# Optimization experiments

Hardware: AMD Instinct MI355X
Metric: run time of the kernel (lower is better)

The kernel has to match this reference:

```python
import jax, jax.numpy as jnp
from jax import lax
import numpy as np

COMMITMENT = 0.25

def conv(x, w, b, stride, pad):
    # x: NCHW, w: OIHW
    y = lax.conv_general_dilated(x, w, (stride, stride), [(pad, pad), (pad, pad)],
                                 dimension_numbers=('NCHW', 'OIHW', 'NCHW'))
    return y + b[None, :, None, None]

def up2(x):
    # PyTorch nn.Upsample(scale_factor=2, mode='bilinear', align_corners=False)
    b, c, h, w = x.shape
    return jax.image.resize(x, (b, c, 2 * h, 2 * w), method='bilinear')

def vq(z, emb):
    # z: (B, D, H, W); emb: (K, D)
    zc = jnp.transpose(z, (0, 2, 3, 1))          # b h w d
    sh = zc.shape
    flat = zc.reshape(-1, sh[-1])                # (N, D)
    dist = (jnp.sum(flat ** 2, axis=1, keepdims=True)
            + jnp.sum(emb ** 2, axis=1)
            - 2.0 * flat @ emb.T)                # (N, K)
    idx = jnp.argmin(dist, axis=1)               # (N,)
    q = emb[idx].reshape(sh)                     # gather == one-hot @ emb
    e_loss = (lax.stop_gradient(q) - zc) ** 2
    q_loss = (q - lax.stop_gradient(zc)) ** 2
    loss = q_loss + COMMITMENT * e_loss          # (b, h, w, d)
    q_st = zc + lax.stop_gradient(q - zc)        # straight-through
    return jnp.transpose(q_st, (0, 3, 1, 2)), loss

def setup_inputs() -> dict:
    key = jax.random.key(0)
    ks = jax.random.split(key, 32)
    S, K, D, IC = 64, 1024, 64, 3
    def w(k, shape, scale=0.05):
        return jax.random.normal(k, shape, jnp.float32) * scale
    z = lambda n: jnp.zeros((n,), jnp.float32)
    return {
        'x': jax.random.normal(ks[0], (8, IC, 256, 256), jnp.float32),
        'ew1': w(ks[1], (S, IC, 3, 3)),        'eb1': z(S),
        'ew2': w(ks[2], (2 * S, S, 3, 3)),     'eb2': z(2 * S),
        'ew3': w(ks[3], (4 * S, 2 * S, 3, 3)), 'eb3': z(4 * S),
        'ew4': w(ks[4], (8 * S, 4 * S, 3, 3)), 'eb4': z(8 * S),
        'pqw': w(ks[5], (D, 8 * S, 1, 1)),     'pqb': z(D),
        'emb': jax.random.uniform(ks[6], (K, D), jnp.float32, -1.0 / K, 1.0 / K),
        'poqw': w(ks[7], (8 * S, D, 1, 1)),    'poqb': z(8 * S),
        'dw1': w(ks[8], (8 * S, 8 * S, 3, 3)), 'db1': z(8 * S),
        'dw2': w(ks[9], (4 * S, 8 * S, 3, 3)), 'db2': z(4 * S),
        'dw3': w(ks[10], (2 * S, 4 * S, 3, 3)),'db3': z(2 * S),
        'dw4': w(ks[11], (S, 2 * S, 3, 3)),    'db4': z(S),
        'ow': w(ks[12], (IC, S, 3, 3)),        'ob': z(IC),
    }

def reference(x, ew1, eb1, ew2, eb2, ew3, eb3, ew4, eb4, pqw, pqb, emb,
              poqw, poqb, dw1, db1, dw2, db2, dw3, db3, dw4, db4, ow, ob):
    silu = jax.nn.silu
    h = silu(conv(x, ew1, eb1, 1, 1))
    h = silu(conv(h, ew2, eb2, 2, 1))
    h = silu(conv(h, ew3, eb3, 2, 1))
    h = conv(h, ew4, eb4, 2, 1)
    zq = conv(h, pqw, pqb, 1, 0)
    q, loss = vq(zq, emb)
    d = conv(q, poqw, poqb, 1, 0)
    d = up2(silu(conv(d, dw1, db1, 1, 1)))
    d = up2(silu(conv(d, dw2, db2, 1, 1)))
    d = up2(silu(conv(d, dw3, db3, 1, 1)))
    d = conv(d, dw4, db4, 1, 1)
    out = jax.nn.sigmoid(conv(d, ow, ob, 1, 1))
    return out, loss
```

## Files before the change

kernel.cpp:

```cpp
#include <hip/hip_runtime.h>
#include <hip/hip_bf16.h>
#include <math.h>

typedef __hip_bfloat16 bf16;
typedef __attribute__((ext_vector_type(8))) short short8;
typedef __attribute__((ext_vector_type(4))) float f32x4;

static __device__ __forceinline__ float bf2f(unsigned short u) {
  return __uint_as_float(((unsigned int)u) << 16);
}
static __device__ __forceinline__ unsigned short f2bf_bits(float f) {
  unsigned int x = __float_as_uint(f);
  x += 0x7fffu + ((x >> 16) & 1u);
  return (unsigned short)(x >> 16);
}
static __device__ __forceinline__ void sto_bf(bf16* p, float v) {
  *reinterpret_cast<unsigned short*>(p) = f2bf_bits(v);
}
struct F4 { float a, b, c, d; };
static __device__ __forceinline__ F4 ld4bf(const bf16* p) {
  uint2 u = *reinterpret_cast<const uint2*>(p);
  return { bf2f((unsigned short)(u.x & 0xffffu)), bf2f((unsigned short)(u.x >> 16)),
           bf2f((unsigned short)(u.y & 0xffffu)), bf2f((unsigned short)(u.y >> 16)) };
}

static __device__ __forceinline__ void g2l16(const void* g, void* l) {
  __builtin_amdgcn_global_load_lds(
      (const __attribute__((address_space(1))) unsigned int*)g,
      (__attribute__((address_space(3))) unsigned int*)l, 16, 0, 0);
}

__global__ __launch_bounds__(256) void wx_toc(const float* __restrict__ src,
                                              bf16* __restrict__ hi, bf16* __restrict__ lo,
                                              int OC, int IC, int T) {
  int total = T * OC * IC;
  int i = blockIdx.x * 256 + threadIdx.x;
  if (i >= total) return;
  int tap = i / (OC * IC); int r = i - tap * OC * IC;
  int oc = r / IC; int ic = r - oc * IC;
  float v = src[(oc * IC + ic) * T + tap];
  float h = bf2f(f2bf_bits(v));
  sto_bf(hi + i, h);
  if (lo) sto_bf(lo + i, v - h);
}
__global__ __launch_bounds__(256) void wx_tico(const float* __restrict__ src,
                                               float* __restrict__ dst,
                                               int OC, int IC, int T) {
  int total = T * OC * IC;
  int i = blockIdx.x * 256 + threadIdx.x;
  if (i >= total) return;
  int tap = i / (IC * OC); int r = i - tap * IC * OC;
  int ic = r / OC; int oc = r - ic * OC;
  dst[i] = src[(oc * IC + ic) * T + tap];
}
__global__ __launch_bounds__(256) void wx_embT(const float* __restrict__ src, float* __restrict__ dst) {
  int i = blockIdx.x * 256 + threadIdx.x;
  if (i >= 65536) return;
  int d = i >> 10, k = i & 1023;
  dst[i] = src[k * 64 + d];
}

__global__ __launch_bounds__(256) void bzero_knl(bf16* __restrict__ buf, int N, int Hp, int Wp, int C) {
  long per = 2 * Wp + 2 * Hp - 4;
  long total = (long)N * per * C;
  long t = (long)blockIdx.x * 256 + threadIdx.x;
  if (t >= total) return;
  int c = (int)(t % C); long q = t / C;
  int pos = (int)(q % per); int n = (int)(q / per);
  int y, x;
  if (pos < Wp) { y = 0; x = pos; }
  else if (pos < 2 * Wp) { y = Hp - 1; x = pos - Wp; }
  else { int r = pos - 2 * Wp; y = 1 + (r >> 1); x = (r & 1) ? Wp - 1 : 0; }
  *reinterpret_cast<unsigned short*>(&buf[(((long)n * Hp + y) * Wp + x) * C + c]) = 0;
}

template <bool SPLIT, int BM, bool TAP9>
__global__ __launch_bounds__(256) void conv_mfma(
    const bf16* __restrict__ inhi, const bf16* __restrict__ inlo,
    int IHp, int IWp, int IC, int kcLog, int stride,
    const bf16* __restrict__ whi, const bf16* __restrict__ wlo,
    const float* __restrict__ bias, int OC, int OH, int OW,
    int omode, int opad, int OHp, int OWp, int silu,
    void* __restrict__ outp, bf16* __restrict__ outlo)
{
  constexpr int NB = SPLIT ? 2 : 1;
  constexpr int AIW = BM / 32;
  constexpr int MREP = 2;
  constexpr int NREP = (BM == 128) ? 4 : 2;
  __shared__ uint4 ldsA[2][NB][BM * 8];
  __shared__ uint4 ldsB[2][NB][64 * 8];

  const int tid = threadIdx.x;
  const int lane = tid & 63;
  const int wv = tid >> 6;
  const int pixBase = blockIdx.x * BM;
  const int ocBase = blockIdx.y * 64;
  const int OHW = OH * OW;

  int aoff[AIW], asl[AIW];
#pragma unroll
  for (int j = 0; j < AIW; ++j) {
    int I = wv * AIW + j;
    int m = I * 8 + (lane >> 3);
    int icoff = ((lane & 7) ^ (m & 7)) * 8;
    int p = pixBase + m;
    int n = p / OHW; int r = p - n * OHW;
    int oy = r / OW; int ox = r - oy * OW;
    aoff[j] = ((n * IHp + oy * stride) * IWp + ox * stride) * IC + icoff;
    asl[j] = I * 64 + lane;
  }
  int boff[2], bsl[2];
#pragma unroll
  for (int j = 0; j < 2; ++j) {
    int I = wv * 2 + j;
    int ocr = I * 8 + (lane >> 3);
    int icoff = ((lane & 7) ^ (ocr & 7)) * 8;
    boff[j] = (ocBase + ocr) * IC + icoff;
    bsl[j] = I * 64 + lane;
  }

  const int kcMask = (1 << kcLog) - 1;
  const int steps = (TAP9 ? 9 : 1) << kcLog;

  auto stage = [&](int buf, int s) {
    int tap = s >> kcLog;
    int k0 = (s & kcMask) << 6;
    int ta = 0;
    if (TAP9) { int ky = tap / 3, kx = tap - ky * 3; ta = (ky * IWp + kx) * IC; }
    int ga = ta + k0;
#pragma unroll
    for (int j = 0; j < AIW; ++j) {
      g2l16(inhi + aoff[j] + ga, &ldsA[buf][0][asl[j]]);
      if constexpr (SPLIT) g2l16(inlo + aoff[j] + ga, &ldsA[buf][1][asl[j]]);
    }
    int gb = tap * OC * IC + k0;
#pragma unroll
    for (int j = 0; j < 2; ++j) {
      g2l16(whi + boff[j] + gb, &ldsB[buf][0][bsl[j]]);
      if constexpr (SPLIT) g2l16(wlo + boff[j] + gb, &ldsB[buf][1][bsl[j]]);
    }
  };

  const int wrow = (BM == 128) ? wv * 32 : (wv >> 1) * 32;
  const int wcol = (BM == 128) ? 0 : (wv & 1) * 32;

  f32x4 acc[MREP][NREP];
#pragma unroll
  for (int i = 0; i < MREP; ++i)
#pragma unroll
    for (int j = 0; j < NREP; ++j) { acc[i][j][0] = 0.f; acc[i][j][1] = 0.f; acc[i][j][2] = 0.f; acc[i][j][3] = 0.f; }

  stage(0, 0);
  __syncthreads();
  int cur = 0;
  for (int s = 0; s < steps; ++s) {
    if (s + 1 < steps) stage(cur ^ 1, s + 1);
#pragma unroll
    for (int kk = 0; kk < 2; ++kk) {
      int kb = kk * 4 + (lane >> 4);
      short8 af[NB][MREP], bfr[NB][NREP];
#pragma unroll
      for (int mr = 0; mr < MREP; ++mr) {
        int row = wrow + mr * 16 + (lane & 15);
        int slot = row * 8 + (kb ^ (row & 7));
        af[0][mr] = *(const short8*)&ldsA[cur][0][slot];
        if constexpr (SPLIT) af[1][mr] = *(const short8*)&ldsA[cur][1][slot];
      }
#pragma unroll
      for (int nr = 0; nr < NREP; ++nr) {
        int ocr = wcol + nr * 16 + (lane & 15);
        int slot = ocr * 8 + (kb ^ (ocr & 7));
        bfr[0][nr] = *(const short8*)&ldsB[cur][0][slot];
        if constexpr (SPLIT) bfr[1][nr] = *(const short8*)&ldsB[cur][1][slot];
      }
#pragma unroll
      for (int mr = 0; mr < MREP; ++mr)
#pragma unroll
        for (int nr = 0; nr < NREP; ++nr) {
          acc[mr][nr] = __builtin_amdgcn_mfma_f32_16x16x32_bf16(af[0][mr], bfr[0][nr], acc[mr][nr], 0, 0, 0);
          if constexpr (SPLIT) {
            acc[mr][nr] = __builtin_amdgcn_mfma_f32_16x16x32_bf16(af[1][mr], bfr[0][nr], acc[mr][nr], 0, 0, 0);
            acc[mr][nr] = __builtin_amdgcn_mfma_f32_16x16x32_bf16(af[0][mr], bfr[1][nr], acc[mr][nr], 0, 0, 0);
          }
        }
    }
    __syncthreads();
    cur ^= 1;
  }

#pragma unroll
  for (int mr = 0; mr < MREP; ++mr) {
#pragma unroll
    for (int nr = 0; nr < NREP; ++nr) {
      int col = ocBase + wcol + nr * 16 + (lane & 15);
      float bv = bias[col];
#pragma unroll
      for (int r = 0; r < 4; ++r) {
        int row = wrow + mr * 16 + (lane >> 4) * 4 + r;
        float v = acc[mr][nr][r] + bv;
        if (silu) v = v / (1.f + expf(-v));
        int p = pixBase + row;
        if (omode == 0) {
          ((float*)outp)[p * OC + col] = v;
        } else {
          int n = p / OHW; int rr = p - n * OHW;
          int oy = rr / OW; int ox = rr - oy * OW;
          int ob = ((n * OHp + oy + opad) * OWp + ox + opad) * OC + col;
          float h = bf2f(f2bf_bits(v));
          sto_bf((bf16*)outp + ob, h);
          if (omode == 2) sto_bf(outlo + ob, v - h);
        }
      }
    }
  }
}

__global__ __launch_bounds__(256) void e1_knl(const float* __restrict__ x,
                                              const float* __restrict__ w,
                                              const float* __restrict__ bias,
                                              bf16* __restrict__ ahi, bf16* __restrict__ alo) {
  int gw = (blockIdx.x << 2) | (threadIdx.x >> 6);
  int lane = threadIdx.x & 63;
  int ox0 = (gw & 63) << 2;
  int oy = (gw >> 6) & 255;
  int n = gw >> 14;

  float wr[27];
#pragma unroll
  for (int j = 0; j < 27; ++j) wr[j] = w[j * 64 + lane];

  float bv = bias[lane];
  float acc[4] = {bv, bv, bv, bv};

#pragma unroll
  for (int ky = 0; ky < 3; ++ky) {
    int iy = oy - 1 + ky;
    if ((unsigned)iy < 256u) {
#pragma unroll
      for (int ic = 0; ic < 3; ++ic) {
        const float* xr = x + ((n * 3 + ic) * 256 + iy) * 256;
        float xv[6];
#pragma unroll
        for (int j = 0; j < 6; ++j) {
          int ix = ox0 - 1 + j;
          xv[j] = ((unsigned)ix < 256u) ? xr[ix] : 0.f;
        }
#pragma unroll
        for (int kx = 0; kx < 3; ++kx) {
          float wv = wr[(ky * 3 + kx) * 3 + ic];
#pragma unroll
          for (int p = 0; p < 4; ++p) acc[p] = fmaf(xv[p + kx], wv, acc[p]);
        }
      }
    }
  }
#pragma unroll
  for (int p = 0; p < 4; ++p) {
    float v = acc[p] / (1.f + __expf(-acc[p]));
    long ob = (((long)n * 258 + oy + 1) * 258 + (ox0 + p + 1)) * 64 + lane;
    float h = bf2f(f2bf_bits(v));
    sto_bf(ahi + ob, h);
    sto_bf(alo + ob, v - h);
  }
}

__global__ __launch_bounds__(256) void up2_knl(const bf16* __restrict__ in, bf16* __restrict__ out,
                                               int N, int H, int W, int C) {
  int C4 = C >> 2;
  int OW = 2 * W, OH = 2 * H;
  long total = (long)N * OH * OW * C4;
  long tid = (long)blockIdx.x * 256 + threadIdx.x;
  if (tid >= total) return;
  int c4 = (int)(tid % C4); long t = tid / C4;
  int ox = (int)(t % OW); t /= OW;
  int oy = (int)(t % OH); int n = (int)(t / OH);
  float sy = 0.5f * oy - 0.25f, sx = 0.5f * ox - 0.25f;
  int y0 = (int)floorf(sy); float fy = sy - (float)y0;
  int x0 = (int)floorf(sx); float fx = sx - (float)x0;
  int y0c = y0 < 0 ? 0 : y0; int y1c = (y0 + 1 > H - 1) ? (H - 1) : (y0 + 1);
  int x0c = x0 < 0 ? 0 : x0; int x1c = (x0 + 1 > W - 1) ? (W - 1) : (x0 + 1);
  const bf16* base = in + (long)n * H * W * C + c4 * 4;
  F4 t00 = ld4bf(base + ((long)y0c * W + x0c) * C);
  F4 t01 = ld4bf(base + ((long)y0c * W + x1c) * C);
  F4 t10 = ld4bf(base + ((long)y1c * W + x0c) * C);
  F4 t11 = ld4bf(base + ((long)y1c * W + x1c) * C);
  float w00 = (1.f - fy) * (1.f - fx), w01 = (1.f - fy) * fx;
  float w10 = fy * (1.f - fx), w11 = fy * fx;
  union { unsigned short us[4]; uint2 u; } pk;
  pk.us[0] = f2bf_bits(w00 * t00.a + w01 * t01.a + w10 * t10.a + w11 * t11.a);
  pk.us[1] = f2bf_bits(w00 * t00.b + w01 * t01.b + w10 * t10.b + w11 * t11.b);
  pk.us[2] = f2bf_bits(w00 * t00.c + w01 * t01.c + w10 * t10.c + w11 * t11.c);
  pk.us[3] = f2bf_bits(w00 * t00.d + w01 * t01.d + w10 * t10.d + w11 * t11.d);
  *reinterpret_cast<uint2*>(out + (((long)n * (OH + 2) + oy + 1) * (OW + 2) + ox + 1) * C + c4 * 4) = pk.u;
}

__global__ __launch_bounds__(256) void vq_knl(const float* __restrict__ zq,
                                              const float* __restrict__ embT,
                                              const float* __restrict__ emb,
                                              bf16* __restrict__ q,
                                              float* __restrict__ loss, int K) {
  __shared__ float z[64];
  __shared__ float sd[256];
  __shared__ int si[256];
  int row = blockIdx.x;
  int tid = threadIdx.x;
  if (tid < 64) z[tid] = zq[(long)row * 64 + tid];
  __syncthreads();
  float best = 3.4e38f; int bi = 0;
  for (int k = tid; k < K; k += 256) {
    float d2 = 0.f;
#pragma unroll
    for (int d = 0; d < 64; ++d) {
      float diff = embT[d * K + k] - z[d];
      d2 = fmaf(diff, diff, d2);
    }
    if (d2 < best) { best = d2; bi = k; }
  }
  sd[tid] = best; si[tid] = bi;
  __syncthreads();
  for (int s = 128; s > 0; s >>= 1) {
    if (tid < s) {
      float od = sd[tid + s]; int oi = si[tid + s];
      if (od < sd[tid] || (od == sd[tid] && oi < si[tid])) { sd[tid] = od; si[tid] = oi; }
    }
    __syncthreads();
  }
  int idx = si[0];
  if (tid < 64) {
    float e = emb[(long)idx * 64 + tid];
    float diff = e - z[tid];
    sto_bf(q + (long)row * 64 + tid, e);
    loss[(long)row * 64 + tid] = 1.25f * diff * diff;
  }
}

__global__ __launch_bounds__(256) void outc_knl(const bf16* __restrict__ in,
                                                const float* __restrict__ w,
                                                const float* __restrict__ bias,
                                                float* __restrict__ out) {
  int pix = blockIdx.x * 256 + threadIdx.x;
  int x = pix & 255;
  int y = (pix >> 8) & 255;
  int n = pix >> 16;
  float a0 = bias[0], a1 = bias[1], a2 = bias[2];
#pragma unroll
  for (int ky = 0; ky < 3; ++ky) {
#pragma unroll
    for (int kx = 0; kx < 3; ++kx) {
      const bf16* ip = in + (((long)(n * 258 + y + ky)) * 258 + (x + kx)) * 64;
      const int t = ky * 3 + kx;
#pragma unroll
      for (int g = 0; g < 8; ++g) {
        short8 v = *reinterpret_cast<const short8*>(ip + g * 8);
#pragma unroll
        for (int j = 0; j < 8; ++j) {
          float f = bf2f((unsigned short)v[j]);
          int ic = g * 8 + j;
          a0 = fmaf(f, w[(t * 64 + ic) * 3 + 0], a0);
          a1 = fmaf(f, w[(t * 64 + ic) * 3 + 1], a1);
          a2 = fmaf(f, w[(t * 64 + ic) * 3 + 2], a2);
        }
      }
    }
  }
  long ob = ((long)n * 3) * 65536 + ((long)y << 8) + x;
  out[ob]          = 1.f / (1.f + __expf(-a0));
  out[ob + 65536]  = 1.f / (1.f + __expf(-a1));
  out[ob + 131072] = 1.f / (1.f + __expf(-a2));
}

extern "C" void kernel_launch(void* const* d_in, const int* in_sizes, int n_in,
                              void* d_out, int out_size, void* d_ws, size_t ws_size,
                              hipStream_t stream) {
  (void)in_sizes; (void)n_in; (void)out_size; (void)ws_size;
  const float* x    = (const float*)d_in[0];
  const float* ew1  = (const float*)d_in[1];  const float* eb1 = (const float*)d_in[2];
  const float* ew2  = (const float*)d_in[3];  const float* eb2 = (const float*)d_in[4];
  const float* ew3  = (const float*)d_in[5];  const float* eb3 = (const float*)d_in[6];
  const float* ew4  = (const float*)d_in[7];  const float* eb4 = (const float*)d_in[8];
  const float* pqw  = (const float*)d_in[9];  const float* pqb = (const float*)d_in[10];
  const float* emb  = (const float*)d_in[11];
  const float* poqw = (const float*)d_in[12]; const float* poqb = (const float*)d_in[13];
  const float* dw1  = (const float*)d_in[14]; const float* db1 = (const float*)d_in[15];
  const float* dw2  = (const float*)d_in[16]; const float* db2 = (const float*)d_in[17];
  const float* dw3  = (const float*)d_in[18]; const float* db3 = (const float*)d_in[19];
  const float* dw4  = (const float*)d_in[20]; const float* db4 = (const float*)d_in[21];
  const float* oww  = (const float*)d_in[22]; const float* ob  = (const float*)d_in[23];

  char* wsb = (char*)d_ws;
  size_t off = 0;
  auto alloc = [&](size_t b) -> char* {
    char* p = wsb + off;
    off = (off + b + 255) & ~(size_t)255;
    return p;
  };

  float* w_e1   = (float*)alloc(1728 * 4);
  float* w_ow   = (float*)alloc(1728 * 4);
  float* w_embT = (float*)alloc(65536 * 4);
  bf16* w_e2h = (bf16*)alloc(73728 * 2);   bf16* w_e2l = (bf16*)alloc(73728 * 2);
  bf16* w_e3h = (bf16*)alloc(294912 * 2);  bf16* w_e3l = (bf16*)alloc(294912 * 2);
  bf16* w_e4h = (bf16*)alloc(1179648 * 2); bf16* w_e4l = (bf16*)alloc(1179648 * 2);
  bf16* w_pqh = (bf16*)alloc(32768 * 2);   bf16* w_pql = (bf16*)alloc(32768 * 2);
  bf16* w_poq = (bf16*)alloc(32768 * 2);
  bf16* w_d1  = (bf16*)alloc(2359296 * 2);
  bf16* w_d2  = (bf16*)alloc(1179648 * 2);
  bf16* w_d3  = (bf16*)alloc(294912 * 2);
  bf16* w_d4  = (bf16*)alloc(73728 * 2);

  char* RA = alloc(68161536);
  char* RB = alloc(68161536);
  char* RC = alloc(28360704);

  bf16* a1h = (bf16*)RA;
  bf16* a1l = (bf16*)(RA + 34080768);
  bf16* u3h_ = (bf16*)RA;

  bf16* a2h = (bf16*)RB;
  bf16* a2l = (bf16*)(RB + 17305600);
  bf16* a3h = (bf16*)(RB + 34611200);
  bf16* a3l = (bf16*)(RB + 43532288);
  bf16* a4h = (bf16*)(RB + 52453376);
  bf16* a4l = (bf16*)(RB + 56647680);
  float* zqH = (float*)(RB + 60841984);

  bf16* u2h_ = (bf16*)RB;
  bf16* c4h_ = (bf16*)RB;
  bf16* c3h_ = (bf16*)(RB + 34611200);
  bf16* c2h_ = (bf16*)(RB + 51388416);
  bf16* c1h_ = (bf16*)(RB + 59777024);

  bf16* qb   = (bf16*)RC;
  bf16* poqO = (bf16*)(RC + 1048576);
  bf16* u1h_ = (bf16*)(RC + 10518528);

  float* out0 = (float*)d_out;
  float* loss = out0 + 1572864;

  auto G1 = [](long n) { return dim3((unsigned)((n + 255) / 256)); };

  wx_tico<<<G1(1728), 256, 0, stream>>>(ew1, w_e1, 64, 3, 9);
  wx_tico<<<G1(1728), 256, 0, stream>>>(oww, w_ow, 3, 64, 9);
  wx_embT<<<G1(65536), 256, 0, stream>>>(emb, w_embT);
  wx_toc<<<G1(73728), 256, 0, stream>>>(ew2, w_e2h, w_e2l, 128, 64, 9);
  wx_toc<<<G1(294912), 256, 0, stream>>>(ew3, w_e3h, w_e3l, 256, 128, 9);
  wx_toc<<<G1(1179648), 256, 0, stream>>>(ew4, w_e4h, w_e4l, 512, 256, 9);
  wx_toc<<<G1(32768), 256, 0, stream>>>(pqw, w_pqh, w_pql, 64, 512, 1);
  wx_toc<<<G1(32768), 256, 0, stream>>>(poqw, w_poq, (bf16*)nullptr, 512, 64, 1);
  wx_toc<<<G1(2359296), 256, 0, stream>>>(dw1, w_d1, (bf16*)nullptr, 512, 512, 9);
  wx_toc<<<G1(1179648), 256, 0, stream>>>(dw2, w_d2, (bf16*)nullptr, 256, 512, 9);
  wx_toc<<<G1(294912), 256, 0, stream>>>(dw3, w_d3, (bf16*)nullptr, 128, 256, 9);
  wx_toc<<<G1(73728), 256, 0, stream>>>(dw4, w_d4, (bf16*)nullptr, 64, 128, 9);

  auto bz = [&](bf16* p, int N, int Hp, int Wp, int C) {
    long tot = (long)N * (2 * Wp + 2 * Hp - 4) * C;
    bzero_knl<<<G1(tot), 256, 0, stream>>>(p, N, Hp, Wp, C);
  };
  bz(a1h, 4, 258, 258, 64); bz(a1l, 4, 258, 258, 64);
  bz(a2h, 4, 130, 130, 128); bz(a2l, 4, 130, 130, 128);
  bz(a3h, 4, 66, 66, 256);   bz(a3l, 4, 66, 66, 256);

  for (int h = 0; h < 2; ++h) {
    const float* xh = x + (size_t)h * 786432;
    e1_knl<<<16384, 256, 0, stream>>>(xh, w_e1, eb1, a1h, a1l);
    conv_mfma<true, 64, true><<<dim3(1024, 2), 256, 0, stream>>>(
        a1h, a1l, 258, 258, 64, 0, 2, w_e2h, w_e2l, eb2, 128, 128, 128, 2, 1, 130, 130, 1, a2h, a2l);
    conv_mfma<true, 64, true><<<dim3(256, 4), 256, 0, stream>>>(
        a2h, a2l, 130, 130, 128, 1, 2, w_e3h, w_e3l, eb3, 256, 64, 64, 2, 1, 66, 66, 1, a3h, a3l);
    conv_mfma<true, 64, true><<<dim3(64, 8), 256, 0, stream>>>(
        a3h, a3l, 66, 66, 256, 2, 2, w_e4h, w_e4l, eb4, 512, 32, 32, 2, 0, 32, 32, 0, a4h, a4l);
    conv_mfma<true, 64, false><<<dim3(64, 1), 256, 0, stream>>>(
        a4h, a4l, 32, 32, 512, 3, 1, w_pqh, w_pql, pqb, 64, 32, 32, 0, 0, 32, 32, 0, zqH, nullptr);
    vq_knl<<<4096, 256, 0, stream>>>(zqH, w_embT, emb, qb + (size_t)h * 262144,
                                     loss + (size_t)h * 262144, 1024);
  }

  bz(poqO, 8, 34, 34, 512);
  bz(u1h_, 4, 66, 66, 512);
  conv_mfma<false, 128, false><<<dim3(64, 8), 256, 0, stream>>>(
      qb, nullptr, 32, 32, 64, 0, 1, w_poq, nullptr, poqb, 512, 32, 32, 1, 1, 34, 34, 0, poqO, nullptr);

  for (int h = 0; h < 2; ++h) {
    bf16* pin = poqO + (size_t)h * 4 * 34 * 34 * 512;
    float* oout = out0 + (size_t)h * 786432;
    conv_mfma<false, 128, true><<<dim3(32, 8), 256, 0, stream>>>(
        pin, nullptr, 34, 34, 512, 3, 1, w_d1, nullptr, db1, 512, 32, 32, 1, 0, 32, 32, 1, c1h_, nullptr);
    up2_knl<<<G1(4l * 64 * 64 * 128), 256, 0, stream>>>(c1h_, u1h_, 4, 32, 32, 512);
    conv_mfma<false, 128, true><<<dim3(128, 4), 256, 0, stream>>>(
        u1h_, nullptr, 66, 66, 512, 3, 1, w_d2, nullptr, db2, 256, 64, 64, 1, 0, 64, 64, 1, c2h_, nullptr);
    bz(u2h_, 4, 130, 130, 256);
    up2_knl<<<G1(4l * 128 * 128 * 64), 256, 0, stream>>>(c2h_, u2h_, 4, 64, 64, 256);
    conv_mfma<false, 128, true><<<dim3(512, 2), 256, 0, stream>>>(
        u2h_, nullptr, 130, 130, 256, 2, 1, w_d3, nullptr, db3, 128, 128, 128, 1, 0, 128, 128, 1, c3h_, nullptr);
    bz(u3h_, 4, 258, 258, 128);
    up2_knl<<<G1(4l * 256 * 256 * 32), 256, 0, stream>>>(c3h_, u3h_, 4, 128, 128, 128);
    bz(c4h_, 4, 258, 258, 64);
    conv_mfma<false, 128, true><<<dim3(2048, 1), 256, 0, stream>>>(
        u3h_, nullptr, 258, 258, 128, 1, 1, w_d4, nullptr, db4, 64, 256, 256, 1, 1, 258, 258, 0, c4h_, nullptr);
    outc_knl<<<1024, 256, 0, stream>>>(c4h_, w_ow, ob, oout);
  }
}
```

Before: 1.585 ms.

## Compute VQ distances as split-bf16 MFMA GEMM plus argmax over scores

Replaces the scalar per-row VQ distance loop with a GEMM formulation. The code scores z·e − ½‖e‖² using the existing split-precision (hi/lo bf16) conv_mfma kernel with a 1x1 tap, then takes a row argmax. The VQ step is batched over both halves at once instead of per half. This moves the 8192×1024×64 distance computation onto matrix cores. In exchange it writes a 32 MB score buffer and adds a split pass, and near-ties could resolve differently than with exact fp32 distances.

```diff
diff --git a/kernel.cpp b/kernel.cpp
--- a/kernel.cpp
+++ b/kernel.cpp
@@ -52,12 +52,6 @@
   int tap = i / (IC * OC); int r = i - tap * IC * OC;
   int ic = r / OC; int oc = r - ic * OC;
   dst[i] = src[(oc * IC + ic) * T + tap];
-}
-__global__ __launch_bounds__(256) void wx_embT(const float* __restrict__ src, float* __restrict__ dst) {
-  int i = blockIdx.x * 256 + threadIdx.x;
-  if (i >= 65536) return;
-  int d = i >> 10, k = i & 1023;
-  dst[i] = src[k * 64 + d];
 }
 
 __global__ __launch_bounds__(256) void bzero_knl(bf16* __restrict__ buf, int N, int Hp, int Wp, int C) {
@@ -294,43 +288,55 @@
   *reinterpret_cast<uint2*>(out + (((long)n * (OH + 2) + oy + 1) * (OW + 2) + ox + 1) * C + c4 * 4) = pk.u;
 }
 
-__global__ __launch_bounds__(256) void vq_knl(const float* __restrict__ zq,
-                                              const float* __restrict__ embT,
-                                              const float* __restrict__ emb,
-                                              bf16* __restrict__ q,
-                                              float* __restrict__ loss, int K) {
-  __shared__ float z[64];
+__global__ __launch_bounds__(256) void zsplit_knl(const float* __restrict__ src,
+                                                  bf16* __restrict__ hi, bf16* __restrict__ lo, int n) {
+  int i = blockIdx.x * 256 + threadIdx.x;
+  if (i >= n) return;
+  float v = src[i];
+  float h = bf2f(f2bf_bits(v));
+  sto_bf(hi + i, h);
+  sto_bf(lo + i, v - h);
+}
+__global__ __launch_bounds__(256) void nbias_knl(const float* __restrict__ emb, float* __restrict__ nb) {
+  int k = blockIdx.x * 256 + threadIdx.x;
+  if (k >= 1024) return;
+  float s = 0.f;
+#pragma unroll
+  for (int d = 0; d < 64; ++d) { float e = emb[k * 64 + d]; s = fmaf(e, e, s); }
+  nb[k] = -0.5f * s;
+}
+__global__ __launch_bounds__(256) void vq2_knl(const float* __restrict__ S,
+                                               const float* __restrict__ zq,
+                                               const float* __restrict__ emb,
+                                               bf16* __restrict__ q, float* __restrict__ loss) {
   __shared__ float sd[256];
   __shared__ int si[256];
   int row = blockIdx.x;
   int tid = threadIdx.x;
-  if (tid < 64) z[tid] = zq[(long)row * 64 + tid];
-  __syncthreads();
-  float best = 3.4e38f; int bi = 0;
-  for (int k = tid; k < K; k += 256) {
-    float d2 = 0.f;
-#pragma unroll
-    for (int d = 0; d < 64; ++d) {
-      float diff = embT[d * K + k] - z[d];
-      d2 = fmaf(diff, diff, d2);
-    }
-    if (d2 < best) { best = d2; bi = k; }
+  const float* Sr = S + (long)row * 1024;
+  float best = -3.4e38f; int bi = 0;
+#pragma unroll
+  for (int j = 0; j < 4; ++j) {
+    int k = tid + j * 256;
+    float v = Sr[k];
+    if (v > best) { best = v; bi = k; }
   }
   sd[tid] = best; si[tid] = bi;
   __syncthreads();
   for (int s = 128; s > 0; s >>= 1) {
     if (tid < s) {
       float od = sd[tid + s]; int oi = si[tid + s];
-      if (od < sd[tid] || (od == sd[tid] && oi < si[tid])) { sd[tid] = od; si[tid] = oi; }
+      if (od > sd[tid] || (od == sd[tid] && oi < si[tid])) { sd[tid] = od; si[tid] = oi; }
     }
     __syncthreads();
   }
   int idx = si[0];
   if (tid < 64) {
     float e = emb[(long)idx * 64 + tid];
-    float diff = e - z[tid];
+    float zv = zq[(long)row * 64 + tid];
+    float d = e - zv;
     sto_bf(q + (long)row * 64 + tid, e);
-    loss[(long)row * 64 + tid] = 1.25f * diff * diff;
+    loss[(long)row * 64 + tid] = 1.25f * d * d;
   }
 }
 
@@ -397,7 +403,8 @@
 
   float* w_e1   = (float*)alloc(1728 * 4);
   float* w_ow   = (float*)alloc(1728 * 4);
-  float* w_embT = (float*)alloc(65536 * 4);
+  float* nbias  = (float*)alloc(1024 * 4);
+  bf16* w_eh  = (bf16*)alloc(65536 * 2);   bf16* w_el  = (bf16*)alloc(65536 * 2);
   bf16* w_e2h = (bf16*)alloc(73728 * 2);   bf16* w_e2l = (bf16*)alloc(73728 * 2);
   bf16* w_e3h = (bf16*)alloc(294912 * 2);  bf16* w_e3l = (bf16*)alloc(294912 * 2);
   bf16* w_e4h = (bf16*)alloc(1179648 * 2); bf16* w_e4l = (bf16*)alloc(1179648 * 2);
@@ -414,6 +421,9 @@
 
   bf16* a1h = (bf16*)RA;
   bf16* a1l = (bf16*)(RA + 34080768);
+  float* Sbuf = (float*)RA;
+  bf16* zqh  = (bf16*)(RA + 33554432);
+  bf16* zql  = (bf16*)(RA + 34603008);
   bf16* u3h_ = (bf16*)RA;
 
   bf16* a2h = (bf16*)RB;
@@ -422,7 +432,7 @@
   bf16* a3l = (bf16*)(RB + 43532288);
   bf16* a4h = (bf16*)(RB + 52453376);
   bf16* a4l = (bf16*)(RB + 56647680);
-  float* zqH = (float*)(RB + 60841984);
+  float* zqF = (float*)(RB + 60841984);
 
   bf16* u2h_ = (bf16*)RB;
   bf16* c4h_ = (bf16*)RB;
@@ -441,7 +451,8 @@
 
   wx_tico<<<G1(1728), 256, 0, stream>>>(ew1, w_e1, 64, 3, 9);
   wx_tico<<<G1(1728), 256, 0, stream>>>(oww, w_ow, 3, 64, 9);
-  wx_embT<<<G1(65536), 256, 0, stream>>>(emb, w_embT);
+  nbias_knl<<<4, 256, 0, stream>>>(emb, nbias);
+  wx_toc<<<G1(65536), 256, 0, stream>>>(emb, w_eh, w_el, 1024, 64, 1);
   wx_toc<<<G1(73728), 256, 0, stream>>>(ew2, w_e2h, w_e2l, 128, 64, 9);
   wx_toc<<<G1(294912), 256, 0, stream>>>(ew3, w_e3h, w_e3l, 256, 128, 9);
   wx_toc<<<G1(1179648), 256, 0, stream>>>(ew4, w_e4h, w_e4l, 512, 256, 9);
@@ -470,10 +481,14 @@
     conv_mfma<true, 64, true><<<dim3(64, 8), 256, 0, stream>>>(
         a3h, a3l, 66, 66, 256, 2, 2, w_e4h, w_e4l, eb4, 512, 32, 32, 2, 0, 32, 32, 0, a4h, a4l);
     conv_mfma<true, 64, false><<<dim3(64, 1), 256, 0, stream>>>(
-        a4h, a4l, 32, 32, 512, 3, 1, w_pqh, w_pql, pqb, 64, 32, 32, 0, 0, 32, 32, 0, zqH, nullptr);
-    vq_knl<<<4096, 256, 0, stream>>>(zqH, w_embT, emb, qb + (size_t)h * 262144,
-                                     loss + (size_t)h * 262144, 1024);
-  }
+        a4h, a4l, 32, 32, 512, 3, 1, w_pqh, w_pql, pqb, 64, 32, 32, 0, 0, 32, 32, 0,
+        zqF + (size_t)h * 262144, nullptr);
+  }
+
+  zsplit_knl<<<G1(524288), 256, 0, stream>>>(zqF, zqh, zql, 524288);
+  conv_mfma<true, 64, false><<<dim3(128, 16), 256, 0, stream>>>(
+      zqh, zql, 32, 32, 64, 0, 1, w_eh, w_el, nbias, 1024, 32, 32, 0, 0, 32, 32, 0, Sbuf, nullptr);
+  vq2_knl<<<8192, 256, 0, stream>>>(Sbuf, zqF, emb, qb, loss);
 
   bz(poqO, 8, 34, 34, 512);
   bz(u1h_, 4, 66, 66, 512);
```

Result: faster. 1.413 ms (-10.9%).
